# Kernel optimization log

Hardware: AMD Instinct MI355X
Metric: run time of the kernel (lower is better)

The kernel has to match this reference:

```python
import jax, jax.numpy as jnp
import numpy as np

B, L, H, NH, F = 32, 200, 256, 4, 2
D = H // NH
C = (2 + F) ** 2  # 16 fused attention streams (queries x keys)
SCALE = np.float32(1.0 / np.sqrt(D))
EPS = 1e-12


def setup_inputs() -> dict:
    key = jax.random.key(0)
    ks = jax.random.split(key, 16)
    p = lambda k, sh: jax.random.normal(k, sh, jnp.float32) * 0.02
    causal = jnp.tril(jnp.ones((L, L), jnp.float32))
    return {
        "input_tensor": jax.random.normal(ks[0], (B, L, H), jnp.float32),
        "attribute_table": jax.random.normal(ks[1], (F, B, L, 1, H), jnp.float32),
        "position_embedding": jax.random.normal(ks[2], (B, L, H), jnp.float32),
        "attention_mask": ((1.0 - causal) * -10000.0)[None, None],  # [1,1,L,L] additive causal mask
        "Wq": p(ks[3], (H, H)), "bq": jnp.zeros((H,), jnp.float32),
        "Wk": p(ks[4], (H, H)), "bk": jnp.zeros((H,), jnp.float32),
        "Wv": p(ks[5], (H, H)), "bv": jnp.zeros((H,), jnp.float32),
        "Wqp": p(ks[6], (H, H)), "bqp": jnp.zeros((H,), jnp.float32),
        "Wkp": p(ks[7], (H, H)), "bkp": jnp.zeros((H,), jnp.float32),
        "Wvp": p(ks[8], (H, H)), "bvp": jnp.zeros((H,), jnp.float32),
        "Wq_a": p(ks[9], (F, H, H)), "bq_a": jnp.zeros((F, H), jnp.float32),
        "Wk_a": p(ks[10], (F, H, H)), "bk_a": jnp.zeros((F, H), jnp.float32),
        "Wv_a": p(ks[11], (F, H, H)), "bv_a": jnp.zeros((F, H), jnp.float32),
        "Wf1": p(ks[12], (L, L)), "bf1": jnp.zeros((L,), jnp.float32),
        "Wf2": p(ks[13], (L, 1)), "bf2": jnp.zeros((1,), jnp.float32),
        "Wd": p(ks[14], (H, H)), "bd": jnp.zeros((H,), jnp.float32),
        "gamma": jnp.ones((H,), jnp.float32),
        "beta": jnp.zeros((H,), jnp.float32),
    }


def _forward(input_tensor, attribute_table, position_embedding, attention_mask,
             Wq, bq, Wk, bk, Wv, bv, Wqp, bqp, Wkp, bkp, Wvp, bvp,
             Wq_a, bq_a, Wk_a, bk_a, Wv_a, bv_a,
             Wf1, bf1, Wf2, bf2, Wd, bd, gamma, beta):
    Bv = input_tensor.shape[0]
    heads = lambda x: x.reshape(Bv, L, NH, D).transpose(0, 2, 1, 3)  # [B,h,L,d]
    q_i = heads(input_tensor @ Wq + bq)
    k_i = heads(input_tensor @ Wk + bk)
    v_i = heads(input_tensor @ Wv + bv)
    q_p = heads(position_embedding @ Wqp + bqp)
    k_p = heads(position_embedding @ Wkp + bkp)
    # NOTE: position values and attribute values are computed by the original module
    # but never consumed (context uses only item values), so we skip them.
    attr = attribute_table[:, :, :, 0, :]  # squeeze(-2) -> [F,B,L,H]
    ah = lambda y: y.reshape(F, Bv, L, NH, D).transpose(0, 1, 3, 2, 4)  # [F,B,h,L,d]
    q_a = ah(jnp.einsum('fblh,fhe->fble', attr, Wq_a) + bq_a[:, None, None, :])
    k_a = ah(jnp.einsum('fblh,fhe->fble', attr, Wk_a) + bk_a[:, None, None, :])
    # query stream order: [item, pos, attr_0..attr_{F-1}]; key order: [item, attr_0..attr_{F-1}, pos]
    Q = jnp.concatenate([q_i[:, None], q_p[:, None], q_a.transpose(1, 0, 2, 3, 4)], axis=1)  # [B,2+F,h,L,d]
    K = jnp.concatenate([k_i[:, None], k_a.transpose(1, 0, 2, 3, 4), k_p[:, None]], axis=1)  # [B,2+F,h,L,d]
    # all query-stream x key-stream raw scores, flattened query-major -> [B,C,h,L,L]
    scores = jnp.einsum('bqhld,bkhmd->bqkhlm', Q, K).reshape(Bv, C, NH, L, L)
    ac = scores.transpose(0, 2, 3, 1, 4)  # [B,h,L,C,L]
    # gate fusion (VanillaAttention over the C stream axis)
    energy = (jax.nn.relu(ac @ Wf1 + bf1) @ Wf2)[..., 0] + bf2  # [B,h,L,C]
    w = jax.nn.softmax(energy, axis=-1)
    attn = jnp.einsum('bhlcm,bhlc->bhlm', ac, w) * SCALE + attention_mask
    probs = jax.nn.softmax(attn, axis=-1)
    ctx = jnp.einsum('bhlm,bhmd->bhld', probs, v_i)
    ctx = ctx.transpose(0, 2, 1, 3).reshape(Bv, L, H)
    x = ctx @ Wd + bd + input_tensor
    mu = x.mean(-1, keepdims=True)
    var = ((x - mu) ** 2).mean(-1, keepdims=True)
    return (x - mu) / jnp.sqrt(var + EPS) * gamma + beta


def reference(input_tensor, attribute_table, position_embedding, attention_mask,
              Wq, bq, Wk, bk, Wv, bv, Wqp, bqp, Wkp, bkp, Wvp, bvp,
              Wq_a, bq_a, Wk_a, bk_a, Wv_a, bv_a,
              Wf1, bf1, Wf2, bf2, Wd, bd, gamma, beta):
    return _forward(input_tensor, attribute_table, position_embedding, attention_mask,
                    Wq, bq, Wk, bk, Wv, bv, Wqp, bqp, Wkp, bkp, Wvp, bvp,
                    Wq_a, bq_a, Wk_a, bk_a, Wv_a, bv_a,
                    Wf1, bf1, Wf2, bf2, Wd, bd, gamma, beta)
```

## Files before the change

### kernel.cpp

```cpp
#include <hip/hip_runtime.h>
#include <hip/hip_bf16.h>

#define B_    32
#define L_    200
#define H_    256
#define NH_   4
#define D_    64
#define SCALE_ 0.125f
#define EPS_  1e-12f

typedef unsigned short u16;
typedef __attribute__((ext_vector_type(8))) short bf16x8;
typedef __attribute__((ext_vector_type(4))) float f32x4;

__device__ __forceinline__ float b2f(u16 u) {
  union { unsigned int i; float f; } v; v.i = ((unsigned int)u) << 16; return v.f;
}
__device__ __forceinline__ u16 f2b(float f) {
  union { float f; unsigned int i; } v; v.f = f;
  unsigned int u = v.i;
  return (u16)((u + 0x7FFF + ((u >> 16) & 1)) >> 16);
}

struct PrepArgs {
  const float* X[4];
  const float* W[10];
  const float* Wf1;
};
struct BiasArgs { const float* Bi[9]; };

__global__ __launch_bounds__(256) void prep_kernel(PrepArgs pa,
    u16* __restrict__ Xb, u16* __restrict__ Wb, u16* __restrict__ Wf1T,
    u16* __restrict__ Qb, u16* __restrict__ Kb) {
  const int N0 = 6553600, N1 = 655360, N2 = 46592, N3 = 786432, N4 = 262144;
  const int total = N0 + N1 + N2 + N3 + N4;
  for (int idx = blockIdx.x * 256 + threadIdx.x; idx < total;
       idx += gridDim.x * 256) {
    if (idx < N0) {
      int i = idx;
      int s = i / 1638400, r = i % 1638400;
      Xb[i] = f2b(pa.X[s][r]);
    } else if (idx < N0 + N1) {
      int i = idx - N0;
      int z = i >> 16, rem = i & 65535, n = rem >> 8, k = rem & 255;
      Wb[i] = f2b(pa.W[z][k * 256 + n]);
    } else if (idx < N0 + N1 + N2) {
      int i = idx - N0 - N1;
      int n = i / 224, m = i % 224;
      Wf1T[i] = (n < 200 && m < 200) ? f2b(pa.Wf1[m * 200 + n]) : (u16)0;
    } else if (idx < N0 + N1 + N2 + N3) {
      int i = idx - N0 - N1 - N2;
      int mat = i / 1536, rr = i % 1536;
      Qb[((size_t)mat * 224 + 200 + rr / 64) * 64 + (rr & 63)] = 0;
    } else {
      int i = idx - N0 - N1 - N2 - N3;
      int mat = i / 512, rr = i % 512;
      Kb[((size_t)mat * 208 + 200 + rr / 64) * 64 + (rr & 63)] = 0;
    }
  }
}

__global__ __launch_bounds__(256) void proj_mfma(
    const u16* __restrict__ Xb, const u16* __restrict__ Wb, BiasArgs ba,
    u16* __restrict__ Qb, u16* __restrict__ Kb, u16* __restrict__ Ktd,
    u16* __restrict__ Vt) {
  const int mb = blockIdx.x, z = blockIdx.y;
  const int row0 = mb * 64;
  const int tid = threadIdx.x;
  const int wv = tid >> 6, ln = tid & 63;
  const int lrow = ln & 15, lk8 = ln >> 4;

  const int zx = (z < 4) ? z : (z == 4 ? 0 : z == 5 ? 2 : z == 6 ? 3 : z == 7 ? 1 : 0);
  const u16* X  = Xb + (size_t)zx * 1638400;
  const u16* Wz = Wb + (size_t)z * 65536;
  const float* bias = ba.Bi[z];

  __shared__ u16 tile[64][264];

  f32x4 c[4][4];
#pragma unroll
  for (int mt = 0; mt < 4; ++mt)
#pragma unroll
    for (int nt = 0; nt < 4; ++nt) c[mt][nt] = (f32x4){0.f, 0.f, 0.f, 0.f};

#pragma unroll
  for (int ks = 0; ks < 8; ++ks) {
    bf16x8 a[4], bfr[4];
#pragma unroll
    for (int mt = 0; mt < 4; ++mt)
      a[mt] = *(const bf16x8*)&X[(size_t)(row0 + mt * 16 + lrow) * 256 + ks * 32 + lk8 * 8];
#pragma unroll
    for (int nt = 0; nt < 4; ++nt)
      bfr[nt] = *(const bf16x8*)&Wz[(size_t)(wv * 64 + nt * 16 + lrow) * 256 + ks * 32 + lk8 * 8];
#pragma unroll
    for (int mt = 0; mt < 4; ++mt)
#pragma unroll
      for (int nt = 0; nt < 4; ++nt)
        c[mt][nt] = __builtin_amdgcn_mfma_f32_16x16x32_bf16(a[mt], bfr[nt], c[mt][nt], 0, 0, 0);
  }

#pragma unroll
  for (int nt = 0; nt < 4; ++nt) {
    int n = wv * 64 + nt * 16 + lrow;
    float bn = bias[n];
#pragma unroll
    for (int mt = 0; mt < 4; ++mt)
#pragma unroll
      for (int j = 0; j < 4; ++j)
        tile[mt * 16 + lk8 * 4 + j][n] = f2b(c[mt][nt][j] + bn);
  }
  __syncthreads();

  if (z < 4) {
    int m = tid >> 2, h = tid & 3;
    int gm = row0 + m, b = gm / 200, l = gm - b * 200;
    u16* dst = &Qb[((size_t)((b * 4 + h) * 4 + z) * 224 + l) * 64];
    const u16* srcp = &tile[m][h * 64];
#pragma unroll
    for (int q = 0; q < 4; ++q)
      *(bf16x8*)&dst[q * 8] = *(const bf16x8*)&srcp[q * 8];
  } else if (z < 8) {
    {
      int m = tid >> 2, h = tid & 3;
      int gm = row0 + m, b = gm / 200, l = gm - b * 200;
      u16* dst = &Kb[((size_t)((b * 4 + h) * 4 + (z - 4)) * 208 + l) * 64];
      const u16* srcp = &tile[m][h * 64];
#pragma unroll
      for (int q = 0; q < 4; ++q)
        *(bf16x8*)&dst[q * 8] = *(const bf16x8*)&srcp[q * 8];
    }
    {
      int h2 = tid >> 6, d = tid & 63;
#pragma unroll
      for (int ch = 0; ch < 8; ++ch) {
        int m0c = ch * 8;
        int gmc = row0 + m0c, bc = gmc / 200, lc = gmc - bc * 200;
        int matc = (bc * 4 + h2) * 4 + (z - 4);
        bf16x8 o;
#pragma unroll
        for (int q = 0; q < 8; ++q) o[q] = (short)tile[m0c + q][h2 * 64 + d];
        *(bf16x8*)&Ktd[((size_t)matc * 64 + d) * 224 + lc] = o;
      }
    }
  } else {
    int h2 = tid >> 6, d = tid & 63;
#pragma unroll
    for (int ch = 0; ch < 8; ++ch) {
      int m0c = ch * 8;
      int gmc = row0 + m0c, bc = gmc / 200, lc = gmc - bc * 200;
      int bhc = bc * 4 + h2;
      bf16x8 o;
#pragma unroll
      for (int q = 0; q < 8; ++q) o[q] = (short)tile[m0c + q][h2 * 64 + d];
      *(bf16x8*)&Vt[((size_t)bhc * 64 + d) * 224 + lc] = o;
    }
  }
}

__global__ __launch_bounds__(256) void kw_mfma(
    const u16* __restrict__ Wf1T, const u16* __restrict__ Ktd,
    u16* __restrict__ KWb) {
  const int mat = blockIdx.x;
  const int tid = threadIdx.x;
  const int wv = tid >> 6, ln = tid & 63;
  const int lrow = ln & 15, lk8 = ln >> 4;
  const u16* Bt = Ktd + (size_t)mat * 64 * 224;

  for (int nt = wv; nt < 13; nt += 4) {
    f32x4 cd0 = {0.f,0.f,0.f,0.f}, cd1 = {0.f,0.f,0.f,0.f};
    f32x4 cd2 = {0.f,0.f,0.f,0.f}, cd3 = {0.f,0.f,0.f,0.f};
#pragma unroll
    for (int ks = 0; ks < 7; ++ks) {
      bf16x8 a = *(const bf16x8*)&Wf1T[(size_t)(nt * 16 + lrow) * 224 + ks * 32 + lk8 * 8];
      bf16x8 b0 = *(const bf16x8*)&Bt[(size_t)(0 * 16 + lrow) * 224 + ks * 32 + lk8 * 8];
      bf16x8 b1 = *(const bf16x8*)&Bt[(size_t)(1 * 16 + lrow) * 224 + ks * 32 + lk8 * 8];
      bf16x8 b2 = *(const bf16x8*)&Bt[(size_t)(2 * 16 + lrow) * 224 + ks * 32 + lk8 * 8];
      bf16x8 b3 = *(const bf16x8*)&Bt[(size_t)(3 * 16 + lrow) * 224 + ks * 32 + lk8 * 8];
      cd0 = __builtin_amdgcn_mfma_f32_16x16x32_bf16(a, b0, cd0, 0, 0, 0);
      cd1 = __builtin_amdgcn_mfma_f32_16x16x32_bf16(a, b1, cd1, 0, 0, 0);
      cd2 = __builtin_amdgcn_mfma_f32_16x16x32_bf16(a, b2, cd2, 0, 0, 0);
      cd3 = __builtin_amdgcn_mfma_f32_16x16x32_bf16(a, b3, cd3, 0, 0, 0);
    }
#pragma unroll
    for (int j = 0; j < 4; ++j) {
      size_t base = ((size_t)mat * 256 + nt * 16 + lk8 * 4 + j) * 64 + lrow;
      KWb[base + 0]  = f2b(cd0[j]);
      KWb[base + 16] = f2b(cd1[j]);
      KWb[base + 32] = f2b(cd2[j]);
      KWb[base + 48] = f2b(cd3[j]);
    }
  }
}

__global__ __launch_bounds__(256) void fused_kernel(
    const u16* __restrict__ Qb, const u16* __restrict__ Kb,
    const u16* __restrict__ KWb, const u16* __restrict__ Vt,
    const float* __restrict__ mask, const float* __restrict__ bf1,
    const float* __restrict__ Wf2, u16* __restrict__ Ctxb) {
  const int bid = blockIdx.x;
  const int wid = (bid & 7) * 112 + (bid >> 3);
  const int lt = wid % 7, bh = wid / 7;
  const int l0 = lt * 32;
  const int b = bh >> 2, h = bh & 3;
  const int tid = threadIdx.x;
  const int wv = tid >> 6, ln = tid & 63;
  const int lrow = ln & 15, lk8 = ln >> 4;

  __shared__ u16  qwpb[8448];
  __shared__ float El[512];
  __shared__ float wg[512];
  __shared__ float b1s[256], w2s[256];
  __shared__ float redm[32][4];
  __shared__ float reds[32][4];

  b1s[tid] = (tid < 200) ? bf1[tid] : 0.f;
  w2s[tid] = (tid < 200) ? Wf2[tid] : 0.f;
  __syncthreads();

  {
    const u16* KWm = KWb + (size_t)(bh * 4 + wv) * 16384;
#pragma unroll
    for (int mt = 0; mt < 2; ++mt) {
      bf16x8 aE[4][2];
#pragma unroll
      for (int cq = 0; cq < 4; ++cq)
#pragma unroll
        for (int ks = 0; ks < 2; ++ks)
          aE[cq][ks] = *(const bf16x8*)&Qb[((size_t)(bh * 4 + cq) * 224 + l0 + mt * 16 + lrow) * 64 + ks * 32 + lk8 * 8];

      f32x4 eacc[4];
#pragma unroll
      for (int cq = 0; cq < 4; ++cq) eacc[cq] = (f32x4){0.f, 0.f, 0.f, 0.f};

      bf16x8 b0 = *(const bf16x8*)&KWm[lrow * 64 + lk8 * 8];
      bf16x8 b1 = *(const bf16x8*)&KWm[lrow * 64 + 32 + lk8 * 8];
#pragma unroll 1
      for (int nt = 0; nt < 13; ++nt) {
        bf16x8 nb0 = b0, nb1 = b1;
        if (nt < 12) {
          nb0 = *(const bf16x8*)&KWm[((nt + 1) * 16 + lrow) * 64 + lk8 * 8];
          nb1 = *(const bf16x8*)&KWm[((nt + 1) * 16 + lrow) * 64 + 32 + lk8 * 8];
        }
        f32x4 c0 = {0.f, 0.f, 0.f, 0.f}, c1 = {0.f, 0.f, 0.f, 0.f};
        f32x4 c2 = {0.f, 0.f, 0.f, 0.f}, c3 = {0.f, 0.f, 0.f, 0.f};
        c0 = __builtin_amdgcn_mfma_f32_16x16x32_bf16(aE[0][0], b0, c0, 0, 0, 0);
        c1 = __builtin_amdgcn_mfma_f32_16x16x32_bf16(aE[1][0], b0, c1, 0, 0, 0);
        c2 = __builtin_amdgcn_mfma_f32_16x16x32_bf16(aE[2][0], b0, c2, 0, 0, 0);
        c3 = __builtin_amdgcn_mfma_f32_16x16x32_bf16(aE[3][0], b0, c3, 0, 0, 0);
        c0 = __builtin_amdgcn_mfma_f32_16x16x32_bf16(aE[0][1], b1, c0, 0, 0, 0);
        c1 = __builtin_amdgcn_mfma_f32_16x16x32_bf16(aE[1][1], b1, c1, 0, 0, 0);
        c2 = __builtin_amdgcn_mfma_f32_16x16x32_bf16(aE[2][1], b1, c2, 0, 0, 0);
        c3 = __builtin_amdgcn_mfma_f32_16x16x32_bf16(aE[3][1], b1, c3, 0, 0, 0);
        float b1n = b1s[nt * 16 + lrow];
        float w2n = w2s[nt * 16 + lrow];
#pragma unroll
        for (int j = 0; j < 4; ++j) {
          eacc[0][j] += fmaxf(c0[j] + b1n, 0.f) * w2n;
          eacc[1][j] += fmaxf(c1[j] + b1n, 0.f) * w2n;
          eacc[2][j] += fmaxf(c2[j] + b1n, 0.f) * w2n;
          eacc[3][j] += fmaxf(c3[j] + b1n, 0.f) * w2n;
        }
        b0 = nb0; b1 = nb1;
      }

#pragma unroll
      for (int cq = 0; cq < 4; ++cq)
#pragma unroll
        for (int j = 0; j < 4; ++j) {
          float v = eacc[cq][j];
          v += __shfl_xor(v, 1);
          v += __shfl_xor(v, 2);
          v += __shfl_xor(v, 4);
          v += __shfl_xor(v, 8);
          if (lrow == 0)
            El[(mt * 16 + lk8 * 4 + j) * 16 + cq * 4 + wv] = v;
        }
    }
  }
  __syncthreads();

#pragma unroll
  for (int it = 0; it < 2; ++it) {
    int l = it * 16 + (tid >> 4), c = tid & 15;
    float e = El[l * 16 + c];
    float mx = e;
    mx = fmaxf(mx, __shfl_xor(mx, 8));
    mx = fmaxf(mx, __shfl_xor(mx, 4));
    mx = fmaxf(mx, __shfl_xor(mx, 2));
    mx = fmaxf(mx, __shfl_xor(mx, 1));
    float ex = __expf(e - mx);
    float s = ex;
    s += __shfl_xor(s, 8);
    s += __shfl_xor(s, 4);
    s += __shfl_xor(s, 2);
    s += __shfl_xor(s, 1);
    wg[l * 16 + c] = ex / s;
  }
  __syncthreads();

  {
    int lq = tid >> 3, d0 = (tid & 7) * 8;
    float qf[4][8];
#pragma unroll
    for (int cq = 0; cq < 4; ++cq) {
      bf16x8 q8 = *(const bf16x8*)&Qb[((size_t)(bh * 4 + cq) * 224 + l0 + lq) * 64 + d0];
#pragma unroll
      for (int j = 0; j < 8; ++j) qf[cq][j] = b2f((u16)q8[j]);
    }
    float wv_[16];
#pragma unroll
    for (int c = 0; c < 16; ++c) wv_[c] = wg[lq * 16 + c];
#pragma unroll
    for (int ck = 0; ck < 4; ++ck) {
      float a[8];
#pragma unroll
      for (int j = 0; j < 8; ++j)
        a[j] = wv_[0 * 4 + ck] * qf[0][j] + wv_[1 * 4 + ck] * qf[1][j] +
               wv_[2 * 4 + ck] * qf[2][j] + wv_[3 * 4 + ck] * qf[3][j];
#pragma unroll
      for (int p = 0; p < 4; ++p) {
        unsigned int pk = f2b(a[2 * p]) | ((unsigned int)f2b(a[2 * p + 1]) << 16);
        *(unsigned int*)&qwpb[lq * 264 + ck * 64 + d0 + 2 * p] = pk;
      }
    }
  }
  __syncthreads();

  f32x4 s0r[4], s1r[4];
#pragma unroll
  for (int q = 0; q < 4; ++q) {
    s0r[q] = (f32x4){0.f, 0.f, 0.f, 0.f};
    s1r[q] = (f32x4){0.f, 0.f, 0.f, 0.f};
  }
#pragma unroll
  for (int q = 0; q < 4; ++q) {
    const int mt = wv + q * 4;
    if (mt < 13) {
      f32x4 sc0 = {0.f, 0.f, 0.f, 0.f}, sc1 = {0.f, 0.f, 0.f, 0.f};
#pragma unroll
      for (int ks = 0; ks < 8; ++ks) {
        int ck = ks >> 1, dd = (ks & 1) * 32 + lk8 * 8;
        const u16* Km = Kb + (size_t)(bh * 4 + ck) * 208 * 64;
        bf16x8 bK = *(const bf16x8*)&Km[(mt * 16 + lrow) * 64 + dd];
        bf16x8 a0 = *(const bf16x8*)&qwpb[lrow * 264 + ck * 64 + dd];
        bf16x8 a1 = *(const bf16x8*)&qwpb[(16 + lrow) * 264 + ck * 64 + dd];
        sc0 = __builtin_amdgcn_mfma_f32_16x16x32_bf16(a0, bK, sc0, 0, 0, 0);
        sc1 = __builtin_amdgcn_mfma_f32_16x16x32_bf16(a1, bK, sc1, 0, 0, 0);
      }
      s0r[q] = sc0; s1r[q] = sc1;
    }
  }

  float e0[4][4], e1[4][4];
#pragma unroll
  for (int q = 0; q < 4; ++q) {
    const int mt = wv + q * 4;
    const int m = mt * 16 + lrow;
#pragma unroll
    for (int j = 0; j < 4; ++j) {
      if (mt < 13 && m < 200) {
        int gla = l0 + lk8 * 4 + j;      if (gla > 199) gla = 199;
        int glb = l0 + 16 + lk8 * 4 + j; if (glb > 199) glb = 199;
        e0[q][j] = s0r[q][j] * SCALE_ + mask[(size_t)gla * 200 + m];
        e1[q][j] = s1r[q][j] * SCALE_ + mask[(size_t)glb * 200 + m];
      } else {
        e0[q][j] = -3.0e38f;
        e1[q][j] = -3.0e38f;
      }
    }
  }
  float M0[4], M1[4];
#pragma unroll
  for (int j = 0; j < 4; ++j) {
    M0[j] = fmaxf(fmaxf(e0[0][j], e0[1][j]), fmaxf(e0[2][j], e0[3][j]));
    M1[j] = fmaxf(fmaxf(e1[0][j], e1[1][j]), fmaxf(e1[2][j], e1[3][j]));
  }
#pragma unroll
  for (int o = 8; o >= 1; o >>= 1)
#pragma unroll
    for (int j = 0; j < 4; ++j) {
      M0[j] = fmaxf(M0[j], __shfl_xor(M0[j], o));
      M1[j] = fmaxf(M1[j], __shfl_xor(M1[j], o));
    }
  if (lrow == 0) {
#pragma unroll
    for (int j = 0; j < 4; ++j) {
      redm[lk8 * 4 + j][wv] = M0[j];
      redm[16 + lk8 * 4 + j][wv] = M1[j];
    }
  }
  __syncthreads();
#pragma unroll
  for (int j = 0; j < 4; ++j) {
    int la = lk8 * 4 + j;
    M0[j] = fmaxf(fmaxf(redm[la][0], redm[la][1]), fmaxf(redm[la][2], redm[la][3]));
    M1[j] = fmaxf(fmaxf(redm[16 + la][0], redm[16 + la][1]),
                  fmaxf(redm[16 + la][2], redm[16 + la][3]));
  }
  float S0[4] = {0.f, 0.f, 0.f, 0.f}, S1[4] = {0.f, 0.f, 0.f, 0.f};
#pragma unroll
  for (int q = 0; q < 4; ++q)
#pragma unroll
    for (int j = 0; j < 4; ++j) {
      e0[q][j] = __expf(e0[q][j] - M0[j]);
      e1[q][j] = __expf(e1[q][j] - M1[j]);
      S0[j] += e0[q][j];
      S1[j] += e1[q][j];
    }
#pragma unroll
  for (int o = 8; o >= 1; o >>= 1)
#pragma unroll
    for (int j = 0; j < 4; ++j) {
      S0[j] += __shfl_xor(S0[j], o);
      S1[j] += __shfl_xor(S1[j], o);
    }
  if (lrow == 0) {
#pragma unroll
    for (int j = 0; j < 4; ++j) {
      reds[lk8 * 4 + j][wv] = S0[j];
      reds[16 + lk8 * 4 + j][wv] = S1[j];
    }
  }
  __syncthreads();
  float R0[4], R1[4];
#pragma unroll
  for (int j = 0; j < 4; ++j) {
    int la = lk8 * 4 + j;
    R0[j] = 1.f / (reds[la][0] + reds[la][1] + reds[la][2] + reds[la][3]);
    R1[j] = 1.f / (reds[16 + la][0] + reds[16 + la][1] +
                   reds[16 + la][2] + reds[16 + la][3]);
  }

  u16* pb = qwpb;
  for (int idx = tid; idx < 768; idx += 256) {
    int l = idx / 24, mm = idx % 24;
    pb[l * 232 + 208 + mm] = 0;
  }
#pragma unroll
  for (int q = 0; q < 4; ++q) {
    const int mt = wv + q * 4;
    if (mt < 13) {
      const int m = mt * 16 + lrow;
#pragma unroll
      for (int j = 0; j < 4; ++j) {
        pb[(lk8 * 4 + j) * 232 + m] = f2b(e0[q][j] * R0[j]);
        pb[(16 + lk8 * 4 + j) * 232 + m] = f2b(e1[q][j] * R1[j]);
      }
    }
  }
  __syncthreads();

  {
    const u16* Vb = Vt + (size_t)bh * 64 * 224;
    f32x4 pc0 = {0.f, 0.f, 0.f, 0.f}, pc1 = {0.f, 0.f, 0.f, 0.f};
#pragma unroll
    for (int ks = 0; ks < 7; ++ks) {
      int mm = ks * 32 + lk8 * 8;
      bf16x8 a0 = *(const bf16x8*)&pb[lrow * 232 + mm];
      bf16x8 a1 = *(const bf16x8*)&pb[(16 + lrow) * 232 + mm];
      bf16x8 bV = *(const bf16x8*)&Vb[(wv * 16 + lrow) * 224 + mm];
      pc0 = __builtin_amdgcn_mfma_f32_16x16x32_bf16(a0, bV, pc0, 0, 0, 0);
      pc1 = __builtin_amdgcn_mfma_f32_16x16x32_bf16(a1, bV, pc1, 0, 0, 0);
    }
#pragma unroll
    for (int j = 0; j < 4; ++j) {
      int la = lk8 * 4 + j, lb = 16 + lk8 * 4 + j;
      int gla = l0 + la, glb = l0 + lb;
      int d = h * 64 + wv * 16 + lrow;
      if (gla < 200) Ctxb[((size_t)b * 200 + gla) * 256 + d] = f2b(pc0[j]);
      if (glb < 200) Ctxb[((size_t)b * 200 + glb) * 256 + d] = f2b(pc1[j]);
    }
  }
}

__global__ __launch_bounds__(256) void out_ln_kernel(
    const u16* __restrict__ Ctxb, const u16* __restrict__ WdT,
    const float* __restrict__ bd, const float* __restrict__ input,
    const float* __restrict__ gamma, const float* __restrict__ beta,
    float* __restrict__ out) {
  const int row0 = blockIdx.x * 32;
  const int tid = threadIdx.x;
  const int wv = tid >> 6, ln = tid & 63;
  const int lrow = ln & 15, lk8 = ln >> 4;

  __shared__ float redA[32][65];
  __shared__ float redB[32][65];
  __shared__ float mus[32], rsd[32];

  f32x4 c[2][4];
#pragma unroll
  for (int mt = 0; mt < 2; ++mt)
#pragma unroll
    for (int nt = 0; nt < 4; ++nt) c[mt][nt] = (f32x4){0.f, 0.f, 0.f, 0.f};

#pragma unroll
  for (int ks = 0; ks < 8; ++ks) {
    bf16x8 a[2], bfr[4];
#pragma unroll
    for (int mt = 0; mt < 2; ++mt)
      a[mt] = *(const bf16x8*)&Ctxb[(size_t)(row0 + mt * 16 + lrow) * 256 + ks * 32 + lk8 * 8];
#pragma unroll
    for (int nt = 0; nt < 4; ++nt)
      bfr[nt] = *(const bf16x8*)&WdT[(size_t)(wv * 64 + nt * 16 + lrow) * 256 + ks * 32 + lk8 * 8];
#pragma unroll
    for (int mt = 0; mt < 2; ++mt)
#pragma unroll
      for (int nt = 0; nt < 4; ++nt)
        c[mt][nt] = __builtin_amdgcn_mfma_f32_16x16x32_bf16(a[mt], bfr[nt], c[mt][nt], 0, 0, 0);
  }

  float s1[2][4], s2[2][4];
#pragma unroll
  for (int mt = 0; mt < 2; ++mt)
#pragma unroll
    for (int j = 0; j < 4; ++j) { s1[mt][j] = 0.f; s2[mt][j] = 0.f; }

#pragma unroll
  for (int nt = 0; nt < 4; ++nt) {
    int n = wv * 64 + nt * 16 + lrow;
    float bdn = bd[n];
#pragma unroll
    for (int mt = 0; mt < 2; ++mt) {
      int mbase = row0 + mt * 16 + lk8 * 4;
#pragma unroll
      for (int j = 0; j < 4; ++j) {
        float x = c[mt][nt][j] + bdn + input[(size_t)(mbase + j) * 256 + n];
        c[mt][nt][j] = x;
        s1[mt][j] += x;
        s2[mt][j] += x * x;
      }
    }
  }
#pragma unroll
  for (int mt = 0; mt < 2; ++mt)
#pragma unroll
    for (int j = 0; j < 4; ++j) {
      redA[mt * 16 + lk8 * 4 + j][wv * 16 + lrow] = s1[mt][j];
      redB[mt * 16 + lk8 * 4 + j][wv * 16 + lrow] = s2[mt][j];
    }
  __syncthreads();
  if (tid < 32) {
    float a = 0.f, b2 = 0.f;
#pragma unroll 8
    for (int i = 0; i < 64; ++i) { a += redA[tid][i]; b2 += redB[tid][i]; }
    float mu = a * (1.f / 256.f);
    float var = b2 * (1.f / 256.f) - mu * mu;
    mus[tid] = mu;
    rsd[tid] = rsqrtf(var + EPS_);
  }
  __syncthreads();
#pragma unroll
  for (int nt = 0; nt < 4; ++nt) {
    int n = wv * 64 + nt * 16 + lrow;
    float g = gamma[n], be = beta[n];
#pragma unroll
    for (int mt = 0; mt < 2; ++mt) {
#pragma unroll
      for (int j = 0; j < 4; ++j) {
        int r = mt * 16 + lk8 * 4 + j;
        out[(size_t)(row0 + r) * 256 + n] = (c[mt][nt][j] - mus[r]) * rsd[r] * g + be;
      }
    }
  }
}

extern "C" void kernel_launch(void* const* d_in, const int* in_sizes, int n_in,
                              void* d_out, int out_size, void* d_ws, size_t ws_size,
                              hipStream_t stream) {
  const float* input = (const float*)d_in[0];
  const float* attrt = (const float*)d_in[1];
  const float* pos   = (const float*)d_in[2];
  const float* mask  = (const float*)d_in[3];
  const float* Wq  = (const float*)d_in[4];   const float* bq  = (const float*)d_in[5];
  const float* Wk  = (const float*)d_in[6];   const float* bk  = (const float*)d_in[7];
  const float* Wv  = (const float*)d_in[8];   const float* bv  = (const float*)d_in[9];
  const float* Wqp = (const float*)d_in[10];  const float* bqp = (const float*)d_in[11];
  const float* Wkp = (const float*)d_in[12];  const float* bkp = (const float*)d_in[13];
  const float* Wq_a = (const float*)d_in[16]; const float* bq_a = (const float*)d_in[17];
  const float* Wk_a = (const float*)d_in[18]; const float* bk_a = (const float*)d_in[19];
  const float* Wf1 = (const float*)d_in[22];  const float* bf1 = (const float*)d_in[23];
  const float* Wf2 = (const float*)d_in[24];
  const float* Wd  = (const float*)d_in[26];  const float* bd  = (const float*)d_in[27];
  const float* gamma = (const float*)d_in[28]; const float* beta = (const float*)d_in[29];

  const float* attr0 = attrt;
  const float* attr1 = attrt + (size_t)B_ * L_ * H_;

  u16* wsu  = (u16*)d_ws;
  u16* Xb   = wsu;
  u16* Wb   = Xb + 6553600;
  u16* Wf1T = Wb + 655360;
  u16* Qb   = Wf1T + 46592;
  u16* Kb   = Qb + 7340032;
  u16* Ktd  = Kb + 6815744;
  u16* Vt   = Ktd + 7340032;
  u16* KWb  = Vt + 1835008;
  u16* Ctxb = KWb + 8388608;

  PrepArgs pp;
  pp.X[0] = input; pp.X[1] = pos; pp.X[2] = attr0; pp.X[3] = attr1;
  pp.W[0] = Wq;  pp.W[1] = Wqp; pp.W[2] = Wq_a; pp.W[3] = Wq_a + 65536;
  pp.W[4] = Wk;  pp.W[5] = Wk_a; pp.W[6] = Wk_a + 65536; pp.W[7] = Wkp;
  pp.W[8] = Wv;  pp.W[9] = Wd;
  pp.Wf1 = Wf1;

  BiasArgs ba;
  ba.Bi[0] = bq;  ba.Bi[1] = bqp;  ba.Bi[2] = bq_a; ba.Bi[3] = bq_a + 256;
  ba.Bi[4] = bk;  ba.Bi[5] = bk_a; ba.Bi[6] = bk_a + 256; ba.Bi[7] = bkp;
  ba.Bi[8] = bv;

  prep_kernel<<<dim3(4096), dim3(256), 0, stream>>>(pp, Xb, Wb, Wf1T, Qb, Kb);
  proj_mfma<<<dim3(100, 9), dim3(256), 0, stream>>>(Xb, Wb, ba, Qb, Kb, Ktd, Vt);
  kw_mfma<<<dim3(512), dim3(256), 0, stream>>>(Wf1T, Ktd, KWb);
  fused_kernel<<<dim3(896), dim3(256), 0, stream>>>(Qb, Kb, KWb, Vt,
                                                    mask, bf1, Wf2, Ctxb);
  out_ln_kernel<<<dim3(200), dim3(256), 0, stream>>>(Ctxb, Wb + 9 * 65536, bd,
                                                     input, gamma, beta,
                                                     (float*)d_out);
}
```

Measured before the change: 138.9 us.

## Double fused attention block to 512 threads, splitting gate N-tiles across wave halves

The fused attention kernel now launches 8 waves per block instead of 4. In the gate-energy stage, the 13 N-tiles are split between two wave groups and their partial energies are summed in shared memory. The score, softmax and Q-weighting stages are redistributed over 8 waves, and only 4 waves do the final PV product. This aims to shorten the per-block serial chain and add latency hiding, at the cost of more registers and LDS pressure per block, lower occupancy per CU, and idle waves in the last stage.

```diff
diff --git a/kernel.cpp b/kernel.cpp
--- a/kernel.cpp
+++ b/kernel.cpp
@@ -11,6 +11,7 @@
 
 typedef unsigned short u16;
 typedef __attribute__((ext_vector_type(8))) short bf16x8;
+typedef __attribute__((ext_vector_type(4))) short bf16x4;
 typedef __attribute__((ext_vector_type(4))) float f32x4;
 
 __device__ __forceinline__ float b2f(u16 u) {
@@ -192,7 +193,7 @@
   }
 }
 
-__global__ __launch_bounds__(256) void fused_kernel(
+__global__ __launch_bounds__(512) void fused_kernel(
     const u16* __restrict__ Qb, const u16* __restrict__ Kb,
     const u16* __restrict__ KWb, const u16* __restrict__ Vt,
     const float* __restrict__ mask, const float* __restrict__ bf1,
@@ -203,22 +204,27 @@
   const int l0 = lt * 32;
   const int b = bh >> 2, h = bh & 3;
   const int tid = threadIdx.x;
-  const int wv = tid >> 6, ln = tid & 63;
+  const int wv8 = tid >> 6, ln = tid & 63;
+  const int ck = wv8 & 3, nh = wv8 >> 2;
   const int lrow = ln & 15, lk8 = ln >> 4;
 
   __shared__ u16  qwpb[8448];
-  __shared__ float El[512];
+  __shared__ float El[2][512];
   __shared__ float wg[512];
   __shared__ float b1s[256], w2s[256];
-  __shared__ float redm[32][4];
-  __shared__ float reds[32][4];
-
-  b1s[tid] = (tid < 200) ? bf1[tid] : 0.f;
-  w2s[tid] = (tid < 200) ? Wf2[tid] : 0.f;
+  __shared__ float redm[32][8];
+  __shared__ float reds[32][8];
+
+  if (tid < 256) {
+    b1s[tid] = (tid < 200) ? bf1[tid] : 0.f;
+    w2s[tid] = (tid < 200) ? Wf2[tid] : 0.f;
+  }
   __syncthreads();
 
   {
-    const u16* KWm = KWb + (size_t)(bh * 4 + wv) * 16384;
+    const u16* KWm = KWb + (size_t)(bh * 4 + ck) * 16384;
+    const int nt0 = nh ? 7 : 0;
+    const int nt1 = nh ? 13 : 7;
 #pragma unroll
     for (int mt = 0; mt < 2; ++mt) {
       bf16x8 aE[4][2];
@@ -232,12 +238,12 @@
 #pragma unroll
       for (int cq = 0; cq < 4; ++cq) eacc[cq] = (f32x4){0.f, 0.f, 0.f, 0.f};
 
-      bf16x8 b0 = *(const bf16x8*)&KWm[lrow * 64 + lk8 * 8];
-      bf16x8 b1 = *(const bf16x8*)&KWm[lrow * 64 + 32 + lk8 * 8];
+      bf16x8 b0 = *(const bf16x8*)&KWm[(nt0 * 16 + lrow) * 64 + lk8 * 8];
+      bf16x8 b1 = *(const bf16x8*)&KWm[(nt0 * 16 + lrow) * 64 + 32 + lk8 * 8];
 #pragma unroll 1
-      for (int nt = 0; nt < 13; ++nt) {
+      for (int nt = nt0; nt < nt1; ++nt) {
         bf16x8 nb0 = b0, nb1 = b1;
-        if (nt < 12) {
+        if (nt + 1 < nt1) {
           nb0 = *(const bf16x8*)&KWm[((nt + 1) * 16 + lrow) * 64 + lk8 * 8];
           nb1 = *(const bf16x8*)&KWm[((nt + 1) * 16 + lrow) * 64 + 32 + lk8 * 8];
         }
@@ -273,16 +279,15 @@
           v += __shfl_xor(v, 4);
           v += __shfl_xor(v, 8);
           if (lrow == 0)
-            El[(mt * 16 + lk8 * 4 + j) * 16 + cq * 4 + wv] = v;
+            El[nh][(mt * 16 + lk8 * 4 + j) * 16 + cq * 4 + ck] = v;
         }
     }
   }
   __syncthreads();
 
-#pragma unroll
-  for (int it = 0; it < 2; ++it) {
-    int l = it * 16 + (tid >> 4), c = tid & 15;
-    float e = El[l * 16 + c];
+  {
+    int l = tid >> 4, c = tid & 15;
+    float e = El[0][l * 16 + c] + El[1][l * 16 + c];
     float mx = e;
     mx = fmaxf(mx, __shfl_xor(mx, 8));
     mx = fmaxf(mx, __shfl_xor(mx, 4));
@@ -299,51 +304,50 @@
   __syncthreads();
 
   {
-    int lq = tid >> 3, d0 = (tid & 7) * 8;
-    float qf[4][8];
+    int lq = tid >> 4, d0 = (tid & 15) * 4;
+    float qf[4][4];
 #pragma unroll
     for (int cq = 0; cq < 4; ++cq) {
-      bf16x8 q8 = *(const bf16x8*)&Qb[((size_t)(bh * 4 + cq) * 224 + l0 + lq) * 64 + d0];
-#pragma unroll
-      for (int j = 0; j < 8; ++j) qf[cq][j] = b2f((u16)q8[j]);
+      bf16x4 q4 = *(const bf16x4*)&Qb[((size_t)(bh * 4 + cq) * 224 + l0 + lq) * 64 + d0];
+#pragma unroll
+      for (int j = 0; j < 4; ++j) qf[cq][j] = b2f((u16)q4[j]);
     }
     float wv_[16];
 #pragma unroll
     for (int c = 0; c < 16; ++c) wv_[c] = wg[lq * 16 + c];
 #pragma unroll
-    for (int ck = 0; ck < 4; ++ck) {
-      float a[8];
-#pragma unroll
-      for (int j = 0; j < 8; ++j)
-        a[j] = wv_[0 * 4 + ck] * qf[0][j] + wv_[1 * 4 + ck] * qf[1][j] +
-               wv_[2 * 4 + ck] * qf[2][j] + wv_[3 * 4 + ck] * qf[3][j];
-#pragma unroll
-      for (int p = 0; p < 4; ++p) {
-        unsigned int pk = f2b(a[2 * p]) | ((unsigned int)f2b(a[2 * p + 1]) << 16);
-        *(unsigned int*)&qwpb[lq * 264 + ck * 64 + d0 + 2 * p] = pk;
-      }
-    }
-  }
-  __syncthreads();
-
-  f32x4 s0r[4], s1r[4];
-#pragma unroll
-  for (int q = 0; q < 4; ++q) {
+    for (int ck4 = 0; ck4 < 4; ++ck4) {
+      float a[4];
+#pragma unroll
+      for (int j = 0; j < 4; ++j)
+        a[j] = wv_[0 * 4 + ck4] * qf[0][j] + wv_[1 * 4 + ck4] * qf[1][j] +
+               wv_[2 * 4 + ck4] * qf[2][j] + wv_[3 * 4 + ck4] * qf[3][j];
+      unsigned int p0 = f2b(a[0]) | ((unsigned int)f2b(a[1]) << 16);
+      unsigned int p1 = f2b(a[2]) | ((unsigned int)f2b(a[3]) << 16);
+      *(unsigned int*)&qwpb[lq * 264 + ck4 * 64 + d0]     = p0;
+      *(unsigned int*)&qwpb[lq * 264 + ck4 * 64 + d0 + 2] = p1;
+    }
+  }
+  __syncthreads();
+
+  f32x4 s0r[2], s1r[2];
+#pragma unroll
+  for (int q = 0; q < 2; ++q) {
     s0r[q] = (f32x4){0.f, 0.f, 0.f, 0.f};
     s1r[q] = (f32x4){0.f, 0.f, 0.f, 0.f};
   }
 #pragma unroll
-  for (int q = 0; q < 4; ++q) {
-    const int mt = wv + q * 4;
+  for (int q = 0; q < 2; ++q) {
+    const int mt = wv8 + q * 8;
     if (mt < 13) {
       f32x4 sc0 = {0.f, 0.f, 0.f, 0.f}, sc1 = {0.f, 0.f, 0.f, 0.f};
 #pragma unroll
       for (int ks = 0; ks < 8; ++ks) {
-        int ck = ks >> 1, dd = (ks & 1) * 32 + lk8 * 8;
-        const u16* Km = Kb + (size_t)(bh * 4 + ck) * 208 * 64;
+        int cks = ks >> 1, dd = (ks & 1) * 32 + lk8 * 8;
+        const u16* Km = Kb + (size_t)(bh * 4 + cks) * 208 * 64;
         bf16x8 bK = *(const bf16x8*)&Km[(mt * 16 + lrow) * 64 + dd];
-        bf16x8 a0 = *(const bf16x8*)&qwpb[lrow * 264 + ck * 64 + dd];
-        bf16x8 a1 = *(const bf16x8*)&qwpb[(16 + lrow) * 264 + ck * 64 + dd];
+        bf16x8 a0 = *(const bf16x8*)&qwpb[lrow * 264 + cks * 64 + dd];
+        bf16x8 a1 = *(const bf16x8*)&qwpb[(16 + lrow) * 264 + cks * 64 + dd];
         sc0 = __builtin_amdgcn_mfma_f32_16x16x32_bf16(a0, bK, sc0, 0, 0, 0);
         sc1 = __builtin_amdgcn_mfma_f32_16x16x32_bf16(a1, bK, sc1, 0, 0, 0);
       }
@@ -351,10 +355,10 @@
     }
   }
 
-  float e0[4][4], e1[4][4];
-#pragma unroll
-  for (int q = 0; q < 4; ++q) {
-    const int mt = wv + q * 4;
+  float e0[2][4], e1[2][4];
+#pragma unroll
+  for (int q = 0; q < 2; ++q) {
+    const int mt = wv8 + q * 8;
     const int m = mt * 16 + lrow;
 #pragma unroll
     for (int j = 0; j < 4; ++j) {
@@ -372,8 +376,8 @@
   float M0[4], M1[4];
 #pragma unroll
   for (int j = 0; j < 4; ++j) {
-    M0[j] = fmaxf(fmaxf(e0[0][j], e0[1][j]), fmaxf(e0[2][j], e0[3][j]));
-    M1[j] = fmaxf(fmaxf(e1[0][j], e1[1][j]), fmaxf(e1[2][j], e1[3][j]));
+    M0[j] = fmaxf(e0[0][j], e0[1][j]);
+    M1[j] = fmaxf(e1[0][j], e1[1][j]);
   }
 #pragma unroll
   for (int o = 8; o >= 1; o >>= 1)
@@ -385,21 +389,25 @@
   if (lrow == 0) {
 #pragma unroll
     for (int j = 0; j < 4; ++j) {
-      redm[lk8 * 4 + j][wv] = M0[j];
-      redm[16 + lk8 * 4 + j][wv] = M1[j];
+      redm[lk8 * 4 + j][wv8] = M0[j];
+      redm[16 + lk8 * 4 + j][wv8] = M1[j];
     }
   }
   __syncthreads();
 #pragma unroll
   for (int j = 0; j < 4; ++j) {
     int la = lk8 * 4 + j;
-    M0[j] = fmaxf(fmaxf(redm[la][0], redm[la][1]), fmaxf(redm[la][2], redm[la][3]));
-    M1[j] = fmaxf(fmaxf(redm[16 + la][0], redm[16 + la][1]),
-                  fmaxf(redm[16 + la][2], redm[16 + la][3]));
+    float m0 = redm[la][0], m1 = redm[16 + la][0];
+#pragma unroll
+    for (int w = 1; w < 8; ++w) {
+      m0 = fmaxf(m0, redm[la][w]);
+      m1 = fmaxf(m1, redm[16 + la][w]);
+    }
+    M0[j] = m0; M1[j] = m1;
   }
   float S0[4] = {0.f, 0.f, 0.f, 0.f}, S1[4] = {0.f, 0.f, 0.f, 0.f};
 #pragma unroll
-  for (int q = 0; q < 4; ++q)
+  for (int q = 0; q < 2; ++q)
 #pragma unroll
     for (int j = 0; j < 4; ++j) {
       e0[q][j] = __expf(e0[q][j] - M0[j]);
@@ -417,8 +425,8 @@
   if (lrow == 0) {
 #pragma unroll
     for (int j = 0; j < 4; ++j) {
-      reds[lk8 * 4 + j][wv] = S0[j];
-      reds[16 + lk8 * 4 + j][wv] = S1[j];
+      reds[lk8 * 4 + j][wv8] = S0[j];
+      reds[16 + lk8 * 4 + j][wv8] = S1[j];
     }
   }
   __syncthreads();
@@ -426,19 +434,24 @@
 #pragma unroll
   for (int j = 0; j < 4; ++j) {
     int la = lk8 * 4 + j;
-    R0[j] = 1.f / (reds[la][0] + reds[la][1] + reds[la][2] + reds[la][3]);
-    R1[j] = 1.f / (reds[16 + la][0] + reds[16 + la][1] +
-                   reds[16 + la][2] + reds[16 + la][3]);
+    float s0 = 0.f, s1v = 0.f;
+#pragma unroll
+    for (int w = 0; w < 8; ++w) {
+      s0 += reds[la][w];
+      s1v += reds[16 + la][w];
+    }
+    R0[j] = 1.f / s0;
+    R1[j] = 1.f / s1v;
   }
 
   u16* pb = qwpb;
-  for (int idx = tid; idx < 768; idx += 256) {
+  for (int idx = tid; idx < 768; idx += 512) {
     int l = idx / 24, mm = idx % 24;
     pb[l * 232 + 208 + mm] = 0;
   }
 #pragma unroll
-  for (int q = 0; q < 4; ++q) {
-    const int mt = wv + q * 4;
+  for (int q = 0; q < 2; ++q) {
+    const int mt = wv8 + q * 8;
     if (mt < 13) {
       const int m = mt * 16 + lrow;
 #pragma unroll
@@ -450,7 +463,7 @@
   }
   __syncthreads();
 
-  {
+  if (wv8 < 4) {
     const u16* Vb = Vt + (size_t)bh * 64 * 224;
     f32x4 pc0 = {0.f, 0.f, 0.f, 0.f}, pc1 = {0.f, 0.f, 0.f, 0.f};
 #pragma unroll
@@ -458,7 +471,7 @@
       int mm = ks * 32 + lk8 * 8;
       bf16x8 a0 = *(const bf16x8*)&pb[lrow * 232 + mm];
       bf16x8 a1 = *(const bf16x8*)&pb[(16 + lrow) * 232 + mm];
-      bf16x8 bV = *(const bf16x8*)&Vb[(wv * 16 + lrow) * 224 + mm];
+      bf16x8 bV = *(const bf16x8*)&Vb[(wv8 * 16 + lrow) * 224 + mm];
       pc0 = __builtin_amdgcn_mfma_f32_16x16x32_bf16(a0, bV, pc0, 0, 0, 0);
       pc1 = __builtin_amdgcn_mfma_f32_16x16x32_bf16(a1, bV, pc1, 0, 0, 0);
     }
@@ -466,7 +479,7 @@
     for (int j = 0; j < 4; ++j) {
       int la = lk8 * 4 + j, lb = 16 + lk8 * 4 + j;
       int gla = l0 + la, glb = l0 + lb;
-      int d = h * 64 + wv * 16 + lrow;
+      int d = h * 64 + wv8 * 16 + lrow;
       if (gla < 200) Ctxb[((size_t)b * 200 + gla) * 256 + d] = f2b(pc0[j]);
       if (glb < 200) Ctxb[((size_t)b * 200 + glb) * 256 + d] = f2b(pc1[j]);
     }
@@ -612,7 +625,7 @@
   prep_kernel<<<dim3(4096), dim3(256), 0, stream>>>(pp, Xb, Wb, Wf1T, Qb, Kb);
   proj_mfma<<<dim3(100, 9), dim3(256), 0, stream>>>(Xb, Wb, ba, Qb, Kb, Ktd, Vt);
   kw_mfma<<<dim3(512), dim3(256), 0, stream>>>(Wf1T, Ktd, KWb);
-  fused_kernel<<<dim3(896), dim3(256), 0, stream>>>(Qb, Kb, KWb, Vt,
+  fused_kernel<<<dim3(896), dim3(512), 0, stream>>>(Qb, Kb, KWb, Vt,
                                                     mask, bf1, Wf2, Ctxb);
   out_ln_kernel<<<dim3(200), dim3(256), 0, stream>>>(Ctxb, Wb + 9 * 65536, bd,
                                                      input, gamma, beta,
```

Result: slower. 156.8 us (+12.9%).
